# Optimization experiments

Measured on AMD Instinct MI355X. Metric: run time of the kernel, lower is better.

Reference implementation:

```python
import jax, jax.numpy as jnp
import numpy as np

S, B, I, H, L = 256, 64, 512, 512, 2
EPS = 1e-5


def _layer_norm(x, g, b):
    m = jnp.mean(x, axis=-1, keepdims=True)
    v = jnp.var(x, axis=-1, keepdims=True)
    return (x - m) * jax.lax.rsqrt(v + EPS) * g + b


def setup_inputs() -> dict:
    key = jax.random.key(0)
    ks = jax.random.split(key, 8)
    gain = float(np.sqrt(1.0 / H))
    inputs = jax.random.normal(ks[0], (S, B, I), dtype=jnp.float32)
    h0 = jnp.zeros((L, B, H), dtype=jnp.float32)
    c0 = jnp.zeros((L, B, H), dtype=jnp.float32)
    # stacked weights (input_size == hidden_size so wx is uniform across layers)
    wx = jax.random.uniform(ks[1], (L, I, 4 * H), minval=-gain, maxval=gain, dtype=jnp.float32)
    wh = jax.random.uniform(ks[2], (L, H, 4 * H), minval=-gain, maxval=gain, dtype=jnp.float32)
    bias = jax.random.uniform(ks[3], (L, 4 * H), minval=-gain, maxval=gain, dtype=jnp.float32)
    # LayerNorm affine params: norm[2l] applied to x@wx, norm[2l+1] applied to h@wh
    ln_gx = jnp.ones((L, 4 * H), dtype=jnp.float32)
    ln_bx = jnp.zeros((L, 4 * H), dtype=jnp.float32)
    ln_gh = jnp.ones((L, 4 * H), dtype=jnp.float32)
    ln_bh = jnp.zeros((L, 4 * H), dtype=jnp.float32)
    return {"inputs": inputs, "h0": h0, "c0": c0, "wx": wx, "wh": wh,
            "bias": bias, "ln_gx": ln_gx, "ln_bx": ln_bx, "ln_gh": ln_gh, "ln_bh": ln_bh}


def reference(inputs, h0, c0, wx, wh, bias, ln_gx, ln_bx, ln_gh, ln_bh):
    x = inputs  # [S, B, I]
    hs, cs = [], []
    for l in range(L):
        # input-to-gate projection + its LayerNorm is time-independent: precompute
        xw = jnp.einsum('sbi,io->sbo', x, wx[l])            # [S, B, 4H]
        xn = _layer_norm(xw, ln_gx[l], ln_bx[l]) + bias[l]  # [S, B, 4H]
        whl, gh, bh = wh[l], ln_gh[l], ln_bh[l]

        def step(carry, xt):
            h, c = carry
            gate = xt + _layer_norm(h @ whl, gh, bh)        # [B, 4H]
            i, f, o, u = jnp.split(gate, 4, axis=-1)
            c = jax.nn.sigmoid(f) * c + jax.nn.sigmoid(i) * jnp.tanh(u)
            h = jax.nn.sigmoid(o) * jnp.tanh(c)
            return (h, c), h

        (hN, cN), ys = jax.lax.scan(step, (h0[l], c0[l]), xn)
        hs.append(hN)
        cs.append(cN)
        x = ys  # [S, B, H]
    h_n = jnp.stack(hs, axis=0)  # [L, B, H]
    c_n = jnp.stack(cs, axis=0)
    return x, h_n, c_n
```

## Files before the change

### kernel.cpp

```cpp
#include <hip/hip_runtime.h>

typedef unsigned short u16;
typedef _Float16 f16;
typedef __attribute__((ext_vector_type(8))) _Float16 f16x8;
typedef __attribute__((ext_vector_type(8))) unsigned short u16x8;
typedef __attribute__((ext_vector_type(4))) float f32x4;

#define NWG 32

__device__ __forceinline__ unsigned split2(float v) {
  f16 h = (f16)v;
  f16 l2 = (f16)((v - (float)h) * 2048.0f);
  return (unsigned)__builtin_bit_cast(u16, h) | ((unsigned)__builtin_bit_cast(u16, l2) << 16);
}

__global__ void k_zero(unsigned long long* __restrict__ ist, unsigned* __restrict__ bar) {
  int tid = threadIdx.x;
  if (tid < 256) ist[tid] = 0ull;
  if (tid < 16) bar[tid] = 0u;
}

__global__ void k_wsplit(const float* __restrict__ wx, u16* __restrict__ th, u16* __restrict__ tl) {
  __shared__ float tile[32][33];
  int l = blockIdx.z;
  int n0 = blockIdx.x * 32, k0 = blockIdx.y * 32;
  int tx = threadIdx.x, ty = threadIdx.y;
  const float* src = wx + (size_t)l * 512 * 2048;
#pragma unroll
  for (int i = 0; i < 4; ++i)
    tile[ty + i * 8][tx] = src[(size_t)(k0 + ty + i * 8) * 2048 + n0 + tx];
  __syncthreads();
  u16* dh = th + (size_t)l * 2048 * 512;
  u16* dl = tl + (size_t)l * 2048 * 512;
#pragma unroll
  for (int i = 0; i < 4; ++i) {
    unsigned s = split2(tile[tx][ty + i * 8]);
    dh[(size_t)(n0 + ty + i * 8) * 512 + k0 + tx] = (u16)s;
    dl[(size_t)(n0 + ty + i * 8) * 512 + k0 + tx] = (u16)(s >> 16);
  }
}

__global__ void k_wlo(const float* __restrict__ wh, u16* __restrict__ wlo) {
  int idx = blockIdx.x * blockDim.x + threadIdx.x;
  int l = idx >> 17;
  int r = idx & 131071;
  int lane = r & 63;
  int fg = r >> 6;
  int kc = fg & 15, q = (fg >> 4) & 3, g = fg >> 6;
  int gcol = g * 16 + (lane & 15) + q * 512;
  int kb = kc * 32 + ((lane >> 4) << 3);
  const float* W = wh + (size_t)l * 512 * 2048;
  u16x8 o;
#pragma unroll
  for (int j = 0; j < 8; ++j)
    o[j] = (u16)(split2(W[(size_t)(kb + j) * 2048 + gcol]) >> 16);
  *(u16x8*)(wlo + (size_t)idx * 8) = o;
}

__global__ void __launch_bounds__(256, 1) k_gemm3(const float* __restrict__ A,
                                                  const u16* __restrict__ Bh, const u16* __restrict__ Bl,
                                                  float* __restrict__ C, int N, int K) {
  __shared__ u16 sA[2][128 * 64];
  __shared__ u16 sB[2][128 * 64];
  const int tid = threadIdx.x, l = tid & 63, w = tid >> 6;
  const int bx = blockIdx.x, by = blockIdx.y;
  const int wr = (w >> 1) * 64, wc = (w & 1) * 64;
  f32x4 acc0[4][4] = {}, acc1[4][4] = {};
  for (int k0 = 0; k0 < K; k0 += 64) {
#pragma unroll
    for (int s = 0; s < 4; ++s) {
      int cn = s * 256 + tid;
      int row = cn >> 3;
      int f0 = (cn & 7) * 8;
      int kb = f0 * 2;
      int sw = row * 128 + (kb ^ ((row & 7) << 4));
      const float* ap = A + ((size_t)(by * 128 + row) * K + k0 + f0);
      float4 a0 = *(const float4*)ap, a1 = *(const float4*)(ap + 4);
      float av[8] = {a0.x, a0.y, a0.z, a0.w, a1.x, a1.y, a1.z, a1.w};
      u16x8 ah_, al_;
#pragma unroll
      for (int j = 0; j < 8; ++j) {
        unsigned sp = split2(av[j]);
        ah_[j] = (u16)sp;
        al_[j] = (u16)(sp >> 16);
      }
      *(u16x8*)((char*)sA[0] + sw) = ah_;
      *(u16x8*)((char*)sA[1] + sw) = al_;
      size_t gb = (((size_t)(bx * 128 + row) * K + k0) << 1) + kb;
      *(u16x8*)((char*)sB[0] + sw) = *(const u16x8*)((const char*)Bh + gb);
      *(u16x8*)((char*)sB[1] + sw) = *(const u16x8*)((const char*)Bl + gb);
    }
    __syncthreads();
#pragma unroll
    for (int kc = 0; kc < 2; ++kc) {
      int kb = kc * 64 + (l >> 4) * 16;
      f16x8 ah[4], al[4], bh[4], bl[4];
#pragma unroll
      for (int mt = 0; mt < 4; ++mt) {
        int row = wr + mt * 16 + (l & 15);
        int off = row * 128 + (kb ^ ((row & 7) << 4));
        ah[mt] = *(const f16x8*)((const char*)sA[0] + off);
        al[mt] = *(const f16x8*)((const char*)sA[1] + off);
      }
#pragma unroll
      for (int nt = 0; nt < 4; ++nt) {
        int col = wc + nt * 16 + (l & 15);
        int off = col * 128 + (kb ^ ((col & 7) << 4));
        bh[nt] = *(const f16x8*)((const char*)sB[0] + off);
        bl[nt] = *(const f16x8*)((const char*)sB[1] + off);
      }
#pragma unroll
      for (int mt = 0; mt < 4; ++mt)
#pragma unroll
        for (int nt = 0; nt < 4; ++nt) {
          acc0[mt][nt] = __builtin_amdgcn_mfma_f32_16x16x32_f16(ah[mt], bh[nt], acc0[mt][nt], 0, 0, 0);
          acc1[mt][nt] = __builtin_amdgcn_mfma_f32_16x16x32_f16(ah[mt], bl[nt], acc1[mt][nt], 0, 0, 0);
          acc1[mt][nt] = __builtin_amdgcn_mfma_f32_16x16x32_f16(al[mt], bh[nt], acc1[mt][nt], 0, 0, 0);
        }
    }
    __syncthreads();
  }
#pragma unroll
  for (int mt = 0; mt < 4; ++mt)
#pragma unroll
    for (int nt = 0; nt < 4; ++nt)
#pragma unroll
      for (int j = 0; j < 4; ++j) {
        int row = by * 128 + wr + mt * 16 + ((l >> 4) << 2) + j;
        int col = bx * 128 + wc + nt * 16 + (l & 15);
        C[(size_t)row * N + col] = acc0[mt][nt][j] + acc1[mt][nt][j] * (1.0f / 2048.0f);
      }
}

__global__ void __launch_bounds__(256) k_ln2(float* __restrict__ X, const float* __restrict__ g,
                                             const float* __restrict__ b, const float* __restrict__ bias) {
  const int row = blockIdx.x, tid = threadIdx.x;
  float* rp = X + (size_t)row * 2048 + tid * 8;
  float4 v0 = *(const float4*)rp, v1 = *(const float4*)(rp + 4);
  float x[8] = {v0.x, v0.y, v0.z, v0.w, v1.x, v1.y, v1.z, v1.w};
  float s1 = 0.f, s2 = 0.f;
#pragma unroll
  for (int j = 0; j < 8; ++j) { s1 += x[j]; s2 += x[j] * x[j]; }
#pragma unroll
  for (int m = 1; m <= 32; m <<= 1) { s1 += __shfl_xor(s1, m, 64); s2 += __shfl_xor(s2, m, 64); }
  __shared__ float a1[4], a2[4];
  if ((tid & 63) == 0) { a1[tid >> 6] = s1; a2[tid >> 6] = s2; }
  __syncthreads();
  s1 = a1[0] + a1[1] + a1[2] + a1[3];
  s2 = a2[0] + a2[1] + a2[2] + a2[3];
  float mu = s1 * (1.f / 2048.f);
  float var = s2 * (1.f / 2048.f) - mu * mu;
  float rstd = 1.0f / sqrtf(var + 1e-5f);
#pragma unroll
  for (int j = 0; j < 8; ++j) {
    int c = tid * 8 + j;
    x[j] = (x[j] - mu) * rstd * g[c] + b[c] + bias[c];
  }
  *(float4*)rp = {x[0], x[1], x[2], x[3]};
  *(float4*)(rp + 4) = {x[4], x[5], x[6], x[7]};
}

__global__ void __launch_bounds__(256, 1) k_scan3(
    const float* __restrict__ wh, const u16* __restrict__ wlo,
    const float* __restrict__ gh, const float* __restrict__ bh,
    const float* __restrict__ xn, const float* __restrict__ h0l, const float* __restrict__ c0l,
    u16* __restrict__ hpubh, u16* __restrict__ hpubl, float* __restrict__ cspill,
    unsigned long long* __restrict__ istats, unsigned* __restrict__ barcnt,
    float* __restrict__ ys, float* __restrict__ hn, float* __restrict__ cn,
    int t0, int first) {
  __shared__ u16 pk[32768];
  const int tid = threadIdx.x;
  const int l = tid & 63, w = tid >> 6;
  const int g = blockIdx.x;
  const int lq = l >> 4, ll = l & 15;
  const int hcol = g * 16 + ll;

  for (int c = tid; c < 4096; c += 256) {
    int lane = c & 63, kc = (c >> 6) & 15, q = c >> 10;
    int gcol = g * 16 + (lane & 15) + q * 512;
    int kb = kc * 32 + ((lane >> 4) << 3);
    u16x8 t8;
#pragma unroll
    for (int j = 0; j < 8; ++j)
      t8[j] = __builtin_bit_cast(u16, (f16)wh[(size_t)(kb + j) * 2048 + gcol]);
    *(u16x8*)(pk + (size_t)c * 8) = t8;
  }
  const u16* wloG = wlo + (size_t)g * 32768;
  float gam[4], bet[4];
#pragma unroll
  for (int q = 0; q < 4; ++q) { int gc = hcol + q * 512; gam[q] = gh[gc]; bet[q] = bh[gc]; }
  float cr[4];
#pragma unroll
  for (int j = 0; j < 4; ++j) {
    int r = w * 16 + lq * 4 + j;
    cr[j] = first ? c0l[r * 512 + hcol] : cspill[r * 512 + hcol];
  }
  if (first) {
    for (int u = tid; u < 1024; u += 256) {
      int row = 2 * g + (u >> 9), col = u & 511;
      unsigned s = split2(h0l[row * 512 + col]);
      hpubh[row * 512 + col] = (u16)s;
      hpubl[row * 512 + col] = (u16)(s >> 16);
    }
  }
  unsigned epoch = 0;
#define GRID_BAR()                                                                           \
  do {                                                                                       \
    epoch++;                                                                                 \
    __syncthreads();                                                                         \
    if (tid == 0) {                                                                          \
      __threadfence();                                                                       \
      __hip_atomic_fetch_add(barcnt, 1u, __ATOMIC_RELAXED, __HIP_MEMORY_SCOPE_AGENT);        \
      while (__hip_atomic_load(barcnt, __ATOMIC_RELAXED, __HIP_MEMORY_SCOPE_AGENT) <         \
             epoch * (unsigned)NWG) {}                                                       \
      __threadfence();                                                                       \
    }                                                                                        \
    __syncthreads();                                                                         \
  } while (0)

  GRID_BAR();

  for (int t = 0; t < 128; ++t) {
    const int p = (t0 + t) & 1;
    float xp[16];
    const float* xrow = xn + (size_t)t * 64 * 2048;
#pragma unroll
    for (int q = 0; q < 4; ++q)
#pragma unroll
      for (int j = 0; j < 4; ++j)
        xp[q * 4 + j] = xrow[(size_t)(w * 16 + lq * 4 + j) * 2048 + hcol + q * 512];

    f32x4 acc0[4] = {}, acc1[4] = {};
#pragma unroll
    for (int kc = 0; kc < 16; ++kc) {
      size_t aoff = (size_t)(w * 16 + ll) * 512 + kc * 32 + lq * 8;
      f16x8 ah = *(const f16x8*)(hpubh + aoff);
      f16x8 al = *(const f16x8*)(hpubl + aoff);
#pragma unroll
      for (int q = 0; q < 4; ++q) {
        f16x8 bhv = *(const f16x8*)(pk + ((size_t)(q * 16 + kc) * 64 + l) * 8);
        f16x8 blv = *(const f16x8*)(wloG + ((size_t)(q * 16 + kc) * 64 + l) * 8);
        acc0[q] = __builtin_amdgcn_mfma_f32_16x16x32_f16(ah, bhv, acc0[q], 0, 0, 0);
        acc1[q] = __builtin_amdgcn_mfma_f32_16x16x32_f16(ah, blv, acc1[q], 0, 0, 0);
        acc1[q] = __builtin_amdgcn_mfma_f32_16x16x32_f16(al, bhv, acc1[q], 0, 0, 0);
      }
    }
    float y[4][4];
#pragma unroll
    for (int q = 0; q < 4; ++q)
#pragma unroll
      for (int j = 0; j < 4; ++j)
        y[q][j] = acc0[q][j] + acc1[q][j] * (1.0f / 2048.0f);

    float s1[4], s2[4];
#pragma unroll
    for (int j = 0; j < 4; ++j) {
      s1[j] = y[0][j] + y[1][j] + y[2][j] + y[3][j];
      s2[j] = y[0][j] * y[0][j] + y[1][j] * y[1][j] + y[2][j] * y[2][j] + y[3][j] * y[3][j];
    }
#pragma unroll
    for (int m = 1; m <= 8; m <<= 1)
#pragma unroll
      for (int j = 0; j < 4; ++j) {
        s1[j] += __shfl_xor(s1[j], m, 64);
        s2[j] += __shfl_xor(s2[j], m, 64);
      }
    if (ll < 8) {
      int j = ll >> 1;
      int r = w * 16 + lq * 4 + j;
      float v = (ll & 1) ? s2[j] : s1[j];
      long long qv = (long long)((double)v * 4294967296.0);
      atomicAdd(&istats[p * 128 + r * 2 + (ll & 1)], (unsigned long long)qv);
    }
    GRID_BAR();
    if (tid < 4)
      __hip_atomic_store(&istats[(1 - p) * 128 + g * 4 + tid], 0ull, __ATOMIC_RELAXED,
                         __HIP_MEMORY_SCOPE_AGENT);
#pragma unroll
    for (int j = 0; j < 4; ++j) {
      int r = w * 16 + lq * 4 + j;
      long long a1 = (long long)__hip_atomic_load(&istats[p * 128 + r * 2], __ATOMIC_RELAXED,
                                                  __HIP_MEMORY_SCOPE_AGENT);
      long long a2 = (long long)__hip_atomic_load(&istats[p * 128 + r * 2 + 1], __ATOMIC_RELAXED,
                                                  __HIP_MEMORY_SCOPE_AGENT);
      float mu = (float)((double)a1 * (1.0 / (4294967296.0 * 2048.0)));
      float ex2 = (float)((double)a2 * (1.0 / (4294967296.0 * 2048.0)));
      float rstd = 1.0f / sqrtf(ex2 - mu * mu + 1e-5f);
      float gv[4];
#pragma unroll
      for (int q = 0; q < 4; ++q)
        gv[q] = (y[q][j] - mu) * rstd * gam[q] + bet[q] + xp[q * 4 + j];
      float fi = 1.f / (1.f + expf(-gv[0]));
      float ff = 1.f / (1.f + expf(-gv[1]));
      float fo = 1.f / (1.f + expf(-gv[2]));
      float fu = tanhf(gv[3]);
      cr[j] = ff * cr[j] + fi * fu;
      float h = fo * tanhf(cr[j]);
      unsigned s = split2(h);
      size_t ro = (size_t)r * 512 + hcol;
      hpubh[ro] = (u16)s;
      hpubl[ro] = (u16)(s >> 16);
      ys[(size_t)t * 32768 + ro] = h;
      if (t == 127) cspill[ro] = cr[j];
      if (t0 + t == 255) { hn[ro] = h; cn[ro] = cr[j]; }
    }
    GRID_BAR();
  }
#undef GRID_BAR
}

#define XN_OFF  0ull
#define WXH_OFF 67108864ull
#define WXL_OFF 71303168ull
#define WLO_OFF 75497472ull
#define HPH_OFF 79691776ull
#define HPL_OFF 79757312ull
#define CSP_OFF 79822848ull
#define IST_OFF 79953920ull
#define BAR_OFF 79955968ull

extern "C" void kernel_launch(void* const* d_in, const int* in_sizes, int n_in,
                              void* d_out, int out_size, void* d_ws, size_t ws_size,
                              hipStream_t stream) {
  const float* inputs = (const float*)d_in[0];
  const float* h0 = (const float*)d_in[1];
  const float* c0 = (const float*)d_in[2];
  const float* wx = (const float*)d_in[3];
  const float* wh = (const float*)d_in[4];
  const float* bias = (const float*)d_in[5];
  const float* gx = (const float*)d_in[6];
  const float* bxp = (const float*)d_in[7];
  const float* ghp = (const float*)d_in[8];
  const float* bhp = (const float*)d_in[9];
  float* out = (float*)d_out;
  char* ws = (char*)d_ws;

  float* xn = (float*)(ws + XN_OFF);
  u16* wxh = (u16*)(ws + WXH_OFF);
  u16* wxl = (u16*)(ws + WXL_OFF);
  u16* wlo = (u16*)(ws + WLO_OFF);
  u16* hph = (u16*)(ws + HPH_OFF);
  u16* hpl = (u16*)(ws + HPL_OFF);
  float* csp = (float*)(ws + CSP_OFF);
  unsigned long long* ist = (unsigned long long*)(ws + IST_OFF);
  unsigned* bar = (unsigned*)(ws + BAR_OFF);

  k_zero<<<1, 256, 0, stream>>>(ist, bar);
  k_wsplit<<<dim3(64, 16, 2), dim3(32, 8), 0, stream>>>(wx, wxh, wxl);
  k_wlo<<<1024, 256, 0, stream>>>(wh, wlo);

  for (int l = 0; l < 2; ++l) {
    const float* Abase = (l == 0) ? inputs : out;
    for (int k = 0; k < 2; ++k) {
      k_gemm3<<<dim3(16, 64), 256, 0, stream>>>(Abase + (size_t)k * 8192 * 512,
                                                wxh + (size_t)l * 2048 * 512,
                                                wxl + (size_t)l * 2048 * 512, xn, 2048, 512);
      k_ln2<<<8192, 256, 0, stream>>>(xn, gx + l * 2048, bxp + l * 2048, bias + l * 2048);
      k_scan3<<<NWG, 256, 0, stream>>>(wh + (size_t)l * 1048576, wlo + (size_t)l * 1048576,
                                       ghp + l * 2048, bhp + l * 2048, xn,
                                       h0 + (size_t)l * 32768, c0 + (size_t)l * 32768,
                                       hph, hpl, csp, ist, bar + (l * 2 + k),
                                       out + (size_t)k * 128 * 32768,
                                       out + 8388608 + (size_t)l * 32768,
                                       out + 8388608 + 65536 + (size_t)l * 32768,
                                       k * 128, (k == 0) ? 1 : 0);
    }
  }
}
```

Measured before the change: 8.583 ms.

## Replace counter grid barrier with per-block flags and pack hidden state

Replaces the single atomic-counter grid barrier with per-workgroup flag slots, each padded to its own cache line. Every block publishes its epoch and polls all 32 flags in parallel, and the xn prefetch is placed between arrive and wait so its loads overlap the barrier. The hi/lo fp16 halves of h are packed into one 32-bit word, so one store publishes both and reads unpack them with byte permutes. LayerNorm stats are loaded once per block into shared memory instead of per thread. The cost is more flag memory, an extra __syncthreads per step, and atomic stores on every output write.

```diff
diff --git a/kernel.cpp b/kernel.cpp
--- a/kernel.cpp
+++ b/kernel.cpp
@@ -5,6 +5,7 @@
 typedef __attribute__((ext_vector_type(8))) _Float16 f16x8;
 typedef __attribute__((ext_vector_type(8))) unsigned short u16x8;
 typedef __attribute__((ext_vector_type(4))) float f32x4;
+typedef __attribute__((ext_vector_type(4))) unsigned u32x4;
 
 #define NWG 32
 
@@ -14,10 +15,10 @@
   return (unsigned)__builtin_bit_cast(u16, h) | ((unsigned)__builtin_bit_cast(u16, l2) << 16);
 }
 
-__global__ void k_zero(unsigned long long* __restrict__ ist, unsigned* __restrict__ bar) {
-  int tid = threadIdx.x;
-  if (tid < 256) ist[tid] = 0ull;
-  if (tid < 16) bar[tid] = 0u;
+__global__ void k_zero(unsigned long long* __restrict__ ist, unsigned* __restrict__ flg) {
+  int i = blockIdx.x * blockDim.x + threadIdx.x;
+  if (i < 256) ist[i] = 0ull;
+  if (i < 8192) flg[i] = 0u;
 }
 
 __global__ void k_wsplit(const float* __restrict__ wx, u16* __restrict__ th, u16* __restrict__ tl) {
@@ -160,15 +161,16 @@
   *(float4*)(rp + 4) = {x[4], x[5], x[6], x[7]};
 }
 
-__global__ void __launch_bounds__(256, 1) k_scan3(
+__global__ void __launch_bounds__(256, 1) k_scan4(
     const float* __restrict__ wh, const u16* __restrict__ wlo,
     const float* __restrict__ gh, const float* __restrict__ bh,
     const float* __restrict__ xn, const float* __restrict__ h0l, const float* __restrict__ c0l,
-    u16* __restrict__ hpubh, u16* __restrict__ hpubl, float* __restrict__ cspill,
-    unsigned long long* __restrict__ istats, unsigned* __restrict__ barcnt,
+    unsigned* __restrict__ hpubp, float* __restrict__ cspill,
+    unsigned long long* __restrict__ istats, unsigned* __restrict__ flags,
     float* __restrict__ ys, float* __restrict__ hn, float* __restrict__ cn,
     int t0, int first) {
   __shared__ u16 pk[32768];
+  __shared__ float musd[128];
   const int tid = threadIdx.x;
   const int l = tid & 63, w = tid >> 6;
   const int g = blockIdx.x;
@@ -198,44 +200,50 @@
   if (first) {
     for (int u = tid; u < 1024; u += 256) {
       int row = 2 * g + (u >> 9), col = u & 511;
-      unsigned s = split2(h0l[row * 512 + col]);
-      hpubh[row * 512 + col] = (u16)s;
-      hpubl[row * 512 + col] = (u16)(s >> 16);
-    }
-  }
-  unsigned epoch = 0;
-#define GRID_BAR()                                                                           \
+      __hip_atomic_store(&hpubp[row * 512 + col], split2(h0l[row * 512 + col]),
+                         __ATOMIC_RELAXED, __HIP_MEMORY_SCOPE_AGENT);
+    }
+  }
+  unsigned bid = 0;
+#define BAR_ARRIVE()                                                                         \
   do {                                                                                       \
-    epoch++;                                                                                 \
+    bid++;                                                                                   \
+    asm volatile("s_waitcnt vmcnt(0)" ::: "memory");                                         \
     __syncthreads();                                                                         \
-    if (tid == 0) {                                                                          \
-      __threadfence();                                                                       \
-      __hip_atomic_fetch_add(barcnt, 1u, __ATOMIC_RELAXED, __HIP_MEMORY_SCOPE_AGENT);        \
-      while (__hip_atomic_load(barcnt, __ATOMIC_RELAXED, __HIP_MEMORY_SCOPE_AGENT) <         \
-             epoch * (unsigned)NWG) {}                                                       \
-      __threadfence();                                                                       \
-    }                                                                                        \
-    __syncthreads();                                                                         \
+    if (tid == 0)                                                                            \
+      __hip_atomic_store(&flags[g * 32], bid, __ATOMIC_RELAXED, __HIP_MEMORY_SCOPE_AGENT);   \
   } while (0)
-
-  GRID_BAR();
+#define BAR_WAIT()                                                                           \
+  do {                                                                                       \
+    if (tid < NWG)                                                                           \
+      while (__hip_atomic_load(&flags[tid * 32], __ATOMIC_RELAXED,                           \
+                               __HIP_MEMORY_SCOPE_AGENT) < bid) {}                           \
+    __builtin_amdgcn_fence(__ATOMIC_ACQUIRE, "agent");                                       \
+  } while (0)
+
+  BAR_ARRIVE();
+  BAR_WAIT();
+  __syncthreads();
 
   for (int t = 0; t < 128; ++t) {
     const int p = (t0 + t) & 1;
-    float xp[16];
-    const float* xrow = xn + (size_t)t * 64 * 2048;
-#pragma unroll
-    for (int q = 0; q < 4; ++q)
-#pragma unroll
-      for (int j = 0; j < 4; ++j)
-        xp[q * 4 + j] = xrow[(size_t)(w * 16 + lq * 4 + j) * 2048 + hcol + q * 512];
-
     f32x4 acc0[4] = {}, acc1[4] = {};
 #pragma unroll
     for (int kc = 0; kc < 16; ++kc) {
-      size_t aoff = (size_t)(w * 16 + ll) * 512 + kc * 32 + lq * 8;
-      f16x8 ah = *(const f16x8*)(hpubh + aoff);
-      f16x8 al = *(const f16x8*)(hpubl + aoff);
+      const unsigned* hp = hpubp + ((size_t)(w * 16 + ll) * 512 + kc * 32 + lq * 8);
+      uint4 pa = *(const uint4*)hp;
+      uint4 pb = *(const uint4*)(hp + 4);
+      u32x4 ahw, alw;
+      ahw[0] = __builtin_amdgcn_perm(pa.y, pa.x, 0x05040100u);
+      ahw[1] = __builtin_amdgcn_perm(pa.w, pa.z, 0x05040100u);
+      ahw[2] = __builtin_amdgcn_perm(pb.y, pb.x, 0x05040100u);
+      ahw[3] = __builtin_amdgcn_perm(pb.w, pb.z, 0x05040100u);
+      alw[0] = __builtin_amdgcn_perm(pa.y, pa.x, 0x07060302u);
+      alw[1] = __builtin_amdgcn_perm(pa.w, pa.z, 0x07060302u);
+      alw[2] = __builtin_amdgcn_perm(pb.y, pb.x, 0x07060302u);
+      alw[3] = __builtin_amdgcn_perm(pb.w, pb.z, 0x07060302u);
+      f16x8 ah = __builtin_bit_cast(f16x8, ahw);
+      f16x8 al = __builtin_bit_cast(f16x8, alw);
 #pragma unroll
       for (int q = 0; q < 4; ++q) {
         f16x8 bhv = *(const f16x8*)(pk + ((size_t)(q * 16 + kc) * 64 + l) * 8);
@@ -272,20 +280,35 @@
       long long qv = (long long)((double)v * 4294967296.0);
       atomicAdd(&istats[p * 128 + r * 2 + (ll & 1)], (unsigned long long)qv);
     }
-    GRID_BAR();
+    BAR_ARRIVE();
+    float xp[16];
+    {
+      const float* xrow = xn + (size_t)t * 64 * 2048;
+#pragma unroll
+      for (int q = 0; q < 4; ++q)
+#pragma unroll
+        for (int j = 0; j < 4; ++j)
+          xp[q * 4 + j] = xrow[(size_t)(w * 16 + lq * 4 + j) * 2048 + hcol + q * 512];
+    }
+    BAR_WAIT();
+    if (tid < 64) {
+      long long a1 = (long long)__hip_atomic_load(&istats[p * 128 + tid * 2], __ATOMIC_RELAXED,
+                                                  __HIP_MEMORY_SCOPE_AGENT);
+      long long a2 = (long long)__hip_atomic_load(&istats[p * 128 + tid * 2 + 1], __ATOMIC_RELAXED,
+                                                  __HIP_MEMORY_SCOPE_AGENT);
+      float mu = (float)((double)a1 * (1.0 / (4294967296.0 * 2048.0)));
+      float ex2 = (float)((double)a2 * (1.0 / (4294967296.0 * 2048.0)));
+      musd[tid] = mu;
+      musd[64 + tid] = 1.0f / sqrtf(ex2 - mu * mu + 1e-5f);
+    }
+    __syncthreads();
     if (tid < 4)
       __hip_atomic_store(&istats[(1 - p) * 128 + g * 4 + tid], 0ull, __ATOMIC_RELAXED,
                          __HIP_MEMORY_SCOPE_AGENT);
 #pragma unroll
     for (int j = 0; j < 4; ++j) {
       int r = w * 16 + lq * 4 + j;
-      long long a1 = (long long)__hip_atomic_load(&istats[p * 128 + r * 2], __ATOMIC_RELAXED,
-                                                  __HIP_MEMORY_SCOPE_AGENT);
-      long long a2 = (long long)__hip_atomic_load(&istats[p * 128 + r * 2 + 1], __ATOMIC_RELAXED,
-                                                  __HIP_MEMORY_SCOPE_AGENT);
-      float mu = (float)((double)a1 * (1.0 / (4294967296.0 * 2048.0)));
-      float ex2 = (float)((double)a2 * (1.0 / (4294967296.0 * 2048.0)));
-      float rstd = 1.0f / sqrtf(ex2 - mu * mu + 1e-5f);
+      float mu = musd[r], rstd = musd[64 + r];
       float gv[4];
 #pragma unroll
       for (int q = 0; q < 4; ++q)
@@ -298,26 +321,31 @@
       float h = fo * tanhf(cr[j]);
       unsigned s = split2(h);
       size_t ro = (size_t)r * 512 + hcol;
-      hpubh[ro] = (u16)s;
-      hpubl[ro] = (u16)(s >> 16);
-      ys[(size_t)t * 32768 + ro] = h;
-      if (t == 127) cspill[ro] = cr[j];
-      if (t0 + t == 255) { hn[ro] = h; cn[ro] = cr[j]; }
-    }
-    GRID_BAR();
-  }
-#undef GRID_BAR
+      __hip_atomic_store(&hpubp[ro], s, __ATOMIC_RELAXED, __HIP_MEMORY_SCOPE_AGENT);
+      __hip_atomic_store(&ys[(size_t)t * 32768 + ro], h, __ATOMIC_RELAXED, __HIP_MEMORY_SCOPE_AGENT);
+      if (t == 127)
+        __hip_atomic_store(&cspill[ro], cr[j], __ATOMIC_RELAXED, __HIP_MEMORY_SCOPE_AGENT);
+      if (t0 + t == 255) {
+        __hip_atomic_store(&hn[ro], h, __ATOMIC_RELAXED, __HIP_MEMORY_SCOPE_AGENT);
+        __hip_atomic_store(&cn[ro], cr[j], __ATOMIC_RELAXED, __HIP_MEMORY_SCOPE_AGENT);
+      }
+    }
+    BAR_ARRIVE();
+    BAR_WAIT();
+    __syncthreads();
+  }
+#undef BAR_ARRIVE
+#undef BAR_WAIT
 }
 
 #define XN_OFF  0ull
 #define WXH_OFF 67108864ull
 #define WXL_OFF 71303168ull
 #define WLO_OFF 75497472ull
-#define HPH_OFF 79691776ull
-#define HPL_OFF 79757312ull
+#define HPP_OFF 79691776ull
 #define CSP_OFF 79822848ull
 #define IST_OFF 79953920ull
-#define BAR_OFF 79955968ull
+#define FLG_OFF 79955968ull
 
 extern "C" void kernel_launch(void* const* d_in, const int* in_sizes, int n_in,
                               void* d_out, int out_size, void* d_ws, size_t ws_size,
@@ -339,13 +367,12 @@
   u16* wxh = (u16*)(ws + WXH_OFF);
   u16* wxl = (u16*)(ws + WXL_OFF);
   u16* wlo = (u16*)(ws + WLO_OFF);
-  u16* hph = (u16*)(ws + HPH_OFF);
-  u16* hpl = (u16*)(ws + HPL_OFF);
+  unsigned* hpp = (unsigned*)(ws + HPP_OFF);
   float* csp = (float*)(ws + CSP_OFF);
   unsigned long long* ist = (unsigned long long*)(ws + IST_OFF);
-  unsigned* bar = (unsigned*)(ws + BAR_OFF);
-
-  k_zero<<<1, 256, 0, stream>>>(ist, bar);
+  unsigned* flg = (unsigned*)(ws + FLG_OFF);
+
+  k_zero<<<32, 256, 0, stream>>>(ist, flg);
   k_wsplit<<<dim3(64, 16, 2), dim3(32, 8), 0, stream>>>(wx, wxh, wxl);
   k_wlo<<<1024, 256, 0, stream>>>(wh, wlo);
 
@@ -356,10 +383,10 @@
                                                 wxh + (size_t)l * 2048 * 512,
                                                 wxl + (size_t)l * 2048 * 512, xn, 2048, 512);
       k_ln2<<<8192, 256, 0, stream>>>(xn, gx + l * 2048, bxp + l * 2048, bias + l * 2048);
-      k_scan3<<<NWG, 256, 0, stream>>>(wh + (size_t)l * 1048576, wlo + (size_t)l * 1048576,
+      k_scan4<<<NWG, 256, 0, stream>>>(wh + (size_t)l * 1048576, wlo + (size_t)l * 1048576,
                                        ghp + l * 2048, bhp + l * 2048, xn,
                                        h0 + (size_t)l * 32768, c0 + (size_t)l * 32768,
-                                       hph, hpl, csp, ist, bar + (l * 2 + k),
+                                       hpp, csp, ist, flg + (size_t)(l * 2 + k) * 2048,
                                        out + (size_t)k * 128 * 32768,
                                        out + 8388608 + (size_t)l * 32768,
                                        out + 8388608 + 65536 + (size_t)l * 32768,
```

Result: faster. 7.427 ms (-13.5%).
